# Kernel tuning notes

Hardware: AMD Instinct MI355X
Metric: run time of the kernel (lower is better)

The kernel has to match this reference:

```python
import jax, jax.numpy as jnp
import numpy as np

ATT_K = 180   # attention_k
NPOOL = 15    # WeldonPooling(15): mean of top-15 + mean of bottom-15 spatial scores


def setup_inputs() -> dict:
    key = jax.random.key(0)
    k1, k2, k3, k4 = jax.random.split(key, 4)
    imgs, emb, h, w = 16, 2400, 14, 14
    caps_cnt = 64
    return {
        "g": jax.random.normal(k1, (imgs, emb, h, w), dtype=jnp.float32),
        "caps": jax.random.normal(k2, (caps_cnt, emb), dtype=jnp.float32),
        "fc_w": jax.random.normal(k3, (emb, emb), dtype=jnp.float32) * 0.02,
        "fc_b": jax.random.normal(k4, (emb,), dtype=jnp.float32) * 0.02,
    }


def reference(g, caps, fc_w, fc_b):
    imgs, emb, h, w = g.shape
    caps_cnt = caps.shape[0]

    # ---- WeldonPooling(15): per (img, channel) sort spatial scores ----
    flat = g.reshape(imgs, emb, h * w)
    s = jnp.sort(flat, axis=2)  # ascending
    hpool = s[:, :, -NPOOL:].mean(axis=2) + s[:, :, :NPOOL].mean(axis=2)  # [imgs, emb]
    x = hpool @ fc_w.T + fc_b  # fc (dropout is identity at eval / p=0)

    # ---- get_heat_map: top-k caption dims, gather fc-projected features ----
    order = jnp.argsort(-caps, axis=1)[:, :ATT_K]                 # [C, k] indices
    vals = jnp.take_along_axis(caps, order, axis=1)               # [C, k] top-k values (desc)
    gf = jnp.einsum('oe,iehw->oihw', fc_w, g)                     # fc.weight @ g -> [emb, imgs, h, w]
    gsel = gf[order]                                              # gather -> [C, k, imgs, h, w]
    heat = jnp.sum(jnp.abs(gsel * vals[:, :, None, None, None]), axis=1)  # [C, imgs, h, w]
    heat = jnp.transpose(heat, (1, 0, 2, 3))                      # [imgs, C, h, w]
    heat = heat / jnp.sum(heat, axis=(2, 3), keepdims=True)       # normalize per (img, cap)

    # ---- attention_embedding: weighted spatial sum, then fc ----
    xa = jnp.einsum('ichw,iehw->ice', heat, g)                    # [imgs, C, emb]
    xa = xa @ fc_w.T + fc_b

    return x, xa, g
```

## Files before the change

kernel.cpp:

```cpp
#include <hip/hip_runtime.h>
#include <math.h>

#define IMGS 16
#define EMB 2400
#define HW 196
#define CAPS 64
#define ATTK 180
#define NPOOL 15
#define NCOLS (IMGS * HW)
#define KPAD 224

typedef __attribute__((ext_vector_type(8))) short short8;
typedef __attribute__((ext_vector_type(4))) float f32x4;
typedef const __attribute__((address_space(1))) unsigned int* gas1_t;
typedef __attribute__((address_space(3))) unsigned int* las3_t;
typedef unsigned long long ull;

__device__ inline unsigned short f2bf(float f) {
    unsigned int u = __builtin_bit_cast(unsigned int, f);
    u += 0x7fffu + ((u >> 16) & 1u);
    return (unsigned short)(u >> 16);
}
__device__ inline float bf2f(unsigned int lo16) {
    return __builtin_bit_cast(float, lo16 << 16);
}
__device__ inline unsigned f2sort(float f) {
    unsigned u = __builtin_bit_cast(unsigned, f);
    int msk = ((int)u) >> 31;
    return u ^ (unsigned)(msk | 0x80000000);
}


__device__ __forceinline__ void transpool_body(char* smem, int bx, int i,
                                               const float* __restrict__ g,
                                               float* __restrict__ hpool,
                                               unsigned short* __restrict__ gT,
                                               float* __restrict__ gout) {
    float(*t)[197] = (float(*)[197])smem;
    int e0 = bx * 32;
    int tid = threadIdx.x;
    const float* base = g + ((size_t)i * EMB + e0) * HW;
    float* obase = gout ? gout + ((size_t)i * EMB + e0) * HW : nullptr;
    for (int f = tid; f < 32 * HW; f += 256) {
        int e = f / HW, hw = f % HW;
        float v = base[(size_t)e * HW + hw];
        t[e][hw] = v;
        if (obase) obase[(size_t)e * HW + hw] = v;
    }
    __syncthreads();
    for (int f = tid; f < HW * 32; f += 256) {
        int hw = f / 32, e = f % 32;
        gT[((size_t)i * HW + hw) * EMB + e0 + e] = f2bf(t[e][hw]);
    }
    int w = tid >> 6, tl = tid & 63, hl = tl & 31;
    bool negh = tl >= 32;
#pragma unroll 1
    for (int rq = 0; rq < 2; ++rq) {
        int eb = w * 8 + rq * 4;
        float s[4][7];
#pragma unroll
        for (int r = 0; r < 4; r++) {
#pragma unroll
            for (int q = 0; q < 7; q++) {
                int hw = hl + 32 * q;
                if (hw < HW) {
                    unsigned u = __builtin_bit_cast(unsigned, t[eb + r][hw]);
                    if (negh) u ^= 0x80000000u;
                    s[r][q] = __builtin_bit_cast(
                        float, (u & 0xFFFFFF00u) | (unsigned)(q * 32 + hl));
                } else {
                    s[r][q] = -INFINITY;
                }
            }
        }
#define CS1(r, a, b)                                       \
    {                                                      \
        float hi = fmaxf(s[r][a], s[r][b]);                \
        float lo = fminf(s[r][a], s[r][b]);                \
        s[r][a] = hi; s[r][b] = lo;                        \
    }
#define CSQ(a, b) CS1(0, a, b) CS1(1, a, b) CS1(2, a, b) CS1(3, a, b)
        CSQ(1, 2) CSQ(3, 4) CSQ(5, 6)
        CSQ(0, 2) CSQ(3, 5) CSQ(4, 6)
        CSQ(0, 1) CSQ(4, 5) CSQ(2, 6)
        CSQ(0, 4) CSQ(1, 5)
        CSQ(0, 3) CSQ(2, 5)
        CSQ(1, 3) CSQ(2, 4)
        CSQ(2, 3)
#undef CSQ
#undef CS1
        float acc[4] = {0.f, 0.f, 0.f, 0.f};
#pragma unroll
        for (int it = 0; it < NPOOL; ++it) {
            int xx[4];
#pragma unroll
            for (int r = 0; r < 4; r++) xx[r] = __builtin_bit_cast(int, s[r][0]);
#define ST4(c)                                                                     \
    {                                                                              \
        _Pragma("unroll") for (int r = 0; r < 4; r++) {                            \
            int y = __builtin_amdgcn_update_dpp(xx[r], xx[r], c, 0xf, 0xf, false); \
            float a = fmaxf(__builtin_bit_cast(float, xx[r]),                      \
                            __builtin_bit_cast(float, y));                         \
            xx[r] = __builtin_bit_cast(int, a);                                    \
        }                                                                          \
    }
            ST4(0x111) ST4(0x112) ST4(0x114) ST4(0x118) ST4(0x142)
#undef ST4
#pragma unroll
            for (int r = 0; r < 4; r++) {
                int m31 = __builtin_amdgcn_readlane(xx[r], 31);
                int m63 = __builtin_amdgcn_readlane(xx[r], 63);
                float msel = __builtin_bit_cast(float, negh ? m63 : m31);
                acc[r] += msel;
                bool won = (__builtin_bit_cast(unsigned, s[r][0]) ==
                            __builtin_bit_cast(unsigned, msel));
                s[r][0] = won ? s[r][1] : s[r][0];
                s[r][1] = won ? s[r][2] : s[r][1];
                s[r][2] = won ? s[r][3] : s[r][2];
                s[r][3] = won ? s[r][4] : s[r][3];
                s[r][4] = won ? s[r][5] : s[r][4];
                s[r][5] = won ? s[r][6] : s[r][5];
                s[r][6] = won ? -INFINITY : s[r][6];
            }
        }
#pragma unroll
        for (int r = 0; r < 4; r++) {
            int ai = __builtin_bit_cast(int, acc[r]);
            float a0 = __builtin_bit_cast(float, __builtin_amdgcn_readlane(ai, 0));
            float a32 = __builtin_bit_cast(float, __builtin_amdgcn_readlane(ai, 32));
            if (tl == 0) hpool[(size_t)i * EMB + e0 + eb + r] = (a0 - a32) / 15.0f;
        }
    }
}

__device__ __forceinline__ void topk_body(char* smem, int c,
                                          const float* __restrict__ caps,
                                          int* __restrict__ idxs,
                                          float* __restrict__ vals) {
    float* rowf = (float*)smem;
    unsigned(*hist)[256] = (unsigned(*)[256])(smem + 9600);
    unsigned* scanbuf = (unsigned*)(smem + 13696);
    unsigned* wtot = (unsigned*)(smem + 14720);
    ull* sprefix = (ull*)(smem + 14744);
    int* srank = (int*)(smem + 14752);
    int tid = threadIdx.x;
    int w = tid >> 6, lane = tid & 63;
    const float4* src = (const float4*)(caps + (size_t)c * EMB);
    for (int j = tid; j < EMB / 4; j += 256) {
        float4 v = src[j];
        *(float4*)&rowf[j * 4] = v;
    }
    if (tid == 0) { *sprefix = 0ull; *srank = ATTK; }
#pragma unroll 1
    for (int pass = 0; pass < 6; ++pass) {
        __syncthreads();
        ull pref = *sprefix;
        int rk = *srank;
        int shift = 40 - pass * 8;
        ull pmaskhi = (pass == 0) ? 0ull : ~((1ull << (shift + 8)) - 1ull);
        hist[0][tid] = 0; hist[1][tid] = 0; hist[2][tid] = 0; hist[3][tid] = 0;
        __syncthreads();
        unsigned* myhist = hist[w];
#pragma unroll 1
        for (int s = 0; s < 10; s++) {
            int e = tid + s * 256;
            if (e < EMB) {
                ull key = ((ull)f2sort(rowf[e]) << 16) | ((unsigned)(2399 - e) << 4);
                if ((key & pmaskhi) == pref)
                    atomicAdd(&myhist[(unsigned)(key >> shift) & 255u], 1u);
            }
        }
        __syncthreads();
        unsigned h = hist[0][tid] + hist[1][tid] + hist[2][tid] + hist[3][tid];
        scanbuf[255 - tid] = h;
        __syncthreads();
        unsigned x = scanbuf[tid];
#pragma unroll
        for (int d = 1; d < 64; d <<= 1) {
            unsigned u = __shfl_up(x, d, 64);
            if (lane >= d) x += u;
        }
        if (lane == 63) wtot[w] = x;
        __syncthreads();
        unsigned off = 0;
        for (int ww = 0; ww < w; ww++) off += wtot[ww];
        scanbuf[tid] = x + off;
        __syncthreads();
        unsigned incl = scanbuf[255 - tid];
        unsigned excl = incl - h;
        if (h > 0u && excl < (unsigned)rk && incl >= (unsigned)rk) {
            *srank = rk - (int)excl;
            *sprefix = pref | ((ull)tid << shift);
        }
    }
    __syncthreads();
    ull T = *sprefix;
    unsigned selmask = 0, cnt = 0;
#pragma unroll 1
    for (int s = 0; s < 10; s++) {
        int e = tid + s * 256;
        if (e < EMB) {
            ull key = ((ull)f2sort(rowf[e]) << 16) | ((unsigned)(2399 - e) << 4);
            if (key >= T) { selmask |= 1u << s; cnt++; }
        }
    }
    unsigned x = cnt;
#pragma unroll
    for (int d = 1; d < 64; d <<= 1) {
        unsigned u = __shfl_up(x, d, 64);
        if (lane >= d) x += u;
    }
    if (lane == 63) wtot[w] = x;
    __syncthreads();
    unsigned off = 0;
    for (int ww = 0; ww < w; ww++) off += wtot[ww];
    unsigned slot = x + off - cnt;
#pragma unroll 1
    for (int s = 0; s < 10; s++) {
        if (selmask & (1u << s)) {
            int e = tid + s * 256;
            idxs[c * ATTK + slot] = e;
            vals[c * ATTK + slot] = fabsf(rowf[e]);
            slot++;
        }
    }
}

__device__ __forceinline__ void convw_body(int b, const float* __restrict__ fc_w,
                                           unsigned short* __restrict__ wbf) {
    int o = b * 4 + (threadIdx.x >> 6);
    int lane = threadIdx.x & 63;
    const float* wrow = fc_w + (size_t)o * EMB;
    unsigned short* wdst = wbf + (size_t)o * EMB;
    for (int e = lane * 4; e < EMB; e += 256) {
        float4 wv = *(const float4*)&wrow[e];
        ushort4 r;
        r.x = f2bf(wv.x); r.y = f2bf(wv.y); r.z = f2bf(wv.z); r.w = f2bf(wv.w);
        *(ushort4*)&wdst[e] = r;
    }
}

__global__ __launch_bounds__(256) void combo_kernel(const float* __restrict__ g,
                                                    float* __restrict__ hpool,
                                                    unsigned short* __restrict__ gT,
                                                    float* __restrict__ gout,
                                                    const float* __restrict__ caps,
                                                    int* __restrict__ idxs,
                                                    float* __restrict__ vals,
                                                    const float* __restrict__ fc_w,
                                                    unsigned short* __restrict__ wbf,
                                                    int nconv) {
    __shared__ __align__(16) char smem[25664];
    int b = blockIdx.x;
    constexpr int NTP = (EMB / 32) * IMGS;
    if (b < NTP) {
        transpool_body(smem, b % (EMB / 32), b / (EMB / 32), g, hpool, gT, gout);
    } else if (b < NTP + nconv) {
        convw_body(b - NTP, fc_w, wbf);
    } else {
        topk_body(smem, b - NTP - nconv, caps, idxs, vals);
    }
}

__global__ void x_kernel(const float* __restrict__ hpool, const float* __restrict__ fc_w,
                         const float* __restrict__ fc_b, float* __restrict__ x_out) {
    int o = blockIdx.x;
    int lane = threadIdx.x;
    float acc[IMGS];
#pragma unroll
    for (int i = 0; i < IMGS; i++) acc[i] = 0.f;
    const float* wrow = fc_w + (size_t)o * EMB;
    for (int e = lane; e < EMB; e += 64) {
        float wv = wrow[e];
#pragma unroll
        for (int i = 0; i < IMGS; i++) acc[i] += hpool[i * EMB + e] * wv;
    }
#pragma unroll
    for (int i = 0; i < IMGS; i++) {
#pragma unroll
        for (int sdx = 32; sdx > 0; sdx >>= 1) acc[i] += __shfl_xor(acc[i], sdx, 64);
    }
    if (lane == 0) {
        float bo = fc_b[o];
#pragma unroll
        for (int i = 0; i < IMGS; i++) x_out[i * EMB + o] = acc[i] + bo;
    }
}

template <int MF, int NF, int OUT_MODE>
__global__ __launch_bounds__(256) void gemm_gll(const unsigned short* __restrict__ A,
                                                const unsigned short* __restrict__ B,
                                                void* __restrict__ outp,
                                                const float* __restrict__ bias,
                                                const float* __restrict__ invS,
                                                int M, int N, int K, int ldb, int kper,
                                                long az, long bz) {
    constexpr int BM = MF * 32, BN = NF * 32;
    constexpr int ROWS = BM + BN;
    constexpr int RPAD = (ROWS + 63) & ~63;
    constexpr int NCALL = RPAD / 16;
    constexpr int LPW = NCALL / 4;
    __shared__ unsigned short lds[3][RPAD][32];
    int gx = gridDim.x, gy = gridDim.y;
    int nwg = gx * gy;
    int flat = blockIdx.y * gx + blockIdx.x;
    int qq = nwg >> 3, rr8 = nwg & 7;
    int xcd = flat & 7, idx = flat >> 3;
    int base = (xcd < rr8) ? xcd * (qq + 1) : rr8 * (qq + 1) + (xcd - rr8) * qq;
    int nf = base + idx;
    int m0 = (nf % gy) * BM;
    int n0 = (nf / gy) * BN;
    int z = blockIdx.z;
    const unsigned short* Ab = A + (size_t)z * az;
    const unsigned short* Bb = B + (size_t)z * bz;
    int kb = (az == 0 && bz == 0) ? z * kper : 0;
    int nt = kper / 32;
    int tid = threadIdx.x, w = tid >> 6, lane = tid & 63;
    int wm = (w >> 1) * (MF * 16), wn = (w & 1) * (NF * 16);
    int ln = lane & 15;
    int ks = (((lane >> 4) ^ ((lane >> 1) & 3))) * 8;
    int srow = lane >> 2;
    int skc = (((lane & 3) ^ ((lane >> 3) & 3))) * 8;

    auto STAGE = [&](int buf, int t) {
        int k0 = kb + t * 32;
#pragma unroll
        for (int j = 0; j < LPW; j++) {
            int jj = w + j * 4;
            int r = jj * 16 + srow;
            const unsigned short* src;
            if (r < BM) src = Ab + (size_t)(m0 + r) * K + k0 + skc;
            else if (r < ROWS) src = Bb + (size_t)(n0 + r - BM) * ldb + k0 + skc;
            else src = Ab + (size_t)m0 * K + k0 + skc;
            __builtin_amdgcn_global_load_lds((gas1_t)(const void*)src,
                                             (las3_t)(void*)&lds[buf][jj * 16][0], 16, 0, 0);
        }
    };

    STAGE(0, 0);
    if (nt > 1) STAGE(1, 1);
    f32x4 acc[MF][NF] = {};
    for (int t = 0; t < nt; ++t) {
        if (t + 1 < nt) {
            if constexpr (LPW == 4) asm volatile("s_waitcnt vmcnt(4) lgkmcnt(0)" ::: "memory");
            else if constexpr (LPW == 5) asm volatile("s_waitcnt vmcnt(5) lgkmcnt(0)" ::: "memory");
            else if constexpr (LPW == 6) asm volatile("s_waitcnt vmcnt(6) lgkmcnt(0)" ::: "memory");
            else asm volatile("s_waitcnt vmcnt(0) lgkmcnt(0)" ::: "memory");
        } else {
            asm volatile("s_waitcnt vmcnt(0) lgkmcnt(0)" ::: "memory");
        }
        __builtin_amdgcn_s_barrier();
        __builtin_amdgcn_sched_barrier(0);
        if (t + 2 < nt) STAGE((t + 2) % 3, t + 2);
        const unsigned short(*buf)[32] = lds[t % 3];
        short8 af[MF], bfv[NF];
#pragma unroll
        for (int mf = 0; mf < MF; mf++)
            af[mf] = *(const short8*)&buf[wm + mf * 16 + ln][ks];
#pragma unroll
        for (int nfi = 0; nfi < NF; nfi++)
            bfv[nfi] = *(const short8*)&buf[BM + wn + nfi * 16 + ln][ks];
        __builtin_amdgcn_s_setprio(1);
#pragma unroll
        for (int mf = 0; mf < MF; mf++)
#pragma unroll
            for (int nfi = 0; nfi < NF; nfi++)
                acc[mf][nfi] = __builtin_amdgcn_mfma_f32_16x16x32_bf16(af[mf], bfv[nfi],
                                                                       acc[mf][nfi], 0, 0, 0);
        __builtin_amdgcn_s_setprio(0);
    }
#pragma unroll
    for (int mf = 0; mf < MF; mf++) {
#pragma unroll
        for (int nfi = 0; nfi < NF; nfi++) {
#pragma unroll
            for (int rr = 0; rr < 4; rr++) {
                int row = m0 + wm + mf * 16 + (lane >> 4) * 4 + rr;
                int col = n0 + wn + nfi * 16 + ln;
                float v = acc[mf][nfi][rr];
                if (OUT_MODE == 6) {
                    ((unsigned short*)outp)[(size_t)row * N + col] = f2bf(v);
                } else if (OUT_MODE == 4) {
                    ((float*)outp)[((size_t)z * CAPS + row) * N + col] =
                        v * invS[z * CAPS + row] + bias[col];
                }
            }
        }
    }
}

__device__ inline uint4 load8(const unsigned short* p) { return *(const uint4*)p; }
__device__ inline uint4 load8(const float* p) {
    float4 a = *(const float4*)p;
    float4 b = *(const float4*)(p + 4);
    uint4 r;
    r.x = (unsigned)f2bf(a.x) | ((unsigned)f2bf(a.y) << 16);
    r.y = (unsigned)f2bf(a.z) | ((unsigned)f2bf(a.w) << 16);
    r.z = (unsigned)f2bf(b.x) | ((unsigned)f2bf(b.y) << 16);
    r.w = (unsigned)f2bf(b.z) | ((unsigned)f2bf(b.w) << 16);
    return r;
}

template <int MF, int NF, typename TA, typename TB>
__global__ __launch_bounds__(256) void mfma_gemm_nt(const TA* __restrict__ A,
                                                    const TB* __restrict__ B,
                                                    void* __restrict__ outp,
                                                    int M, int N, int K) {
    constexpr int BM = MF * 32, BN = NF * 32;
    constexpr int nA = BM * 4, nTot = (BM + BN) * 4;
    constexpr int NCH = (nTot + 255) / 256;
    __shared__ unsigned short As[BM][40];
    __shared__ unsigned short Bs[BN][40];
    int m0 = blockIdx.y * BM, n0 = blockIdx.x * BN;
    int tid = threadIdx.x;
    int w = tid >> 6, lane = tid & 63;
    int wm = (w >> 1) * (MF * 16), wn = (w & 1) * (NF * 16);
    int ln = lane & 15, ks = (lane >> 4) * 8;
    uint4 r[NCH];
#pragma unroll
    for (int j = 0; j < NCH; j++) {
        int c = tid + 256 * j;
        if (c < nTot) {
            if (c < nA) {
                int row = c >> 2, kc = c & 3;
                r[j] = load8(A + (size_t)(m0 + row) * K + kc * 8);
            } else {
                int cc = c - nA, row = cc >> 2, kc = cc & 3;
                r[j] = load8(B + (size_t)(n0 + row) * K + kc * 8);
            }
        }
    }
    f32x4 acc[MF][NF] = {};
    for (int k0 = 0; k0 < K; k0 += 32) {
#pragma unroll
        for (int j = 0; j < NCH; j++) {
            int c = tid + 256 * j;
            if (c < nTot) {
                if (c < nA) {
                    int row = c >> 2, kc = c & 3;
                    *(uint4*)&As[row][kc * 8] = r[j];
                } else {
                    int cc = c - nA, row = cc >> 2, kc = cc & 3;
                    *(uint4*)&Bs[row][kc * 8] = r[j];
                }
            }
        }
        __syncthreads();
        if (k0 + 32 < K) {
#pragma unroll
            for (int j = 0; j < NCH; j++) {
                int c = tid + 256 * j;
                if (c < nTot) {
                    if (c < nA) {
                        int row = c >> 2, kc = c & 3;
                        r[j] = load8(A + (size_t)(m0 + row) * K + (k0 + 32) + kc * 8);
                    } else {
                        int cc = c - nA, row = cc >> 2, kc = cc & 3;
                        r[j] = load8(B + (size_t)(n0 + row) * K + (k0 + 32) + kc * 8);
                    }
                }
            }
        }
        short8 af[MF], bfv[NF];
#pragma unroll
        for (int mf = 0; mf < MF; mf++)
            af[mf] = *(const short8*)&As[wm + mf * 16 + ln][ks];
#pragma unroll
        for (int nfi = 0; nfi < NF; nfi++)
            bfv[nfi] = *(const short8*)&Bs[wn + nfi * 16 + ln][ks];
#pragma unroll
        for (int mf = 0; mf < MF; mf++)
#pragma unroll
            for (int nfi = 0; nfi < NF; nfi++)
                acc[mf][nfi] = __builtin_amdgcn_mfma_f32_16x16x32_bf16(af[mf], bfv[nfi],
                                                                       acc[mf][nfi], 0, 0, 0);
        __syncthreads();
    }
#pragma unroll
    for (int mf = 0; mf < MF; mf++) {
#pragma unroll
        for (int nfi = 0; nfi < NF; nfi++) {
#pragma unroll
            for (int rr = 0; rr < 4; rr++) {
                int row = m0 + wm + mf * 16 + (lane >> 4) * 4 + rr;
                int col = n0 + wn + nfi * 16 + ln;
                ((unsigned short*)outp)[(size_t)row * N + col] = f2bf(acc[mf][nfi][rr]);
            }
        }
    }
}

__global__ __launch_bounds__(256) void heatx_kernel(const int* __restrict__ idxs,
                                                    const float* __restrict__ vals,
                                                    const unsigned short* __restrict__ A,
                                                    unsigned short* __restrict__ Hnbf,
                                                    float* __restrict__ invS,
                                                    const float* __restrict__ hpool,
                                                    const unsigned short* __restrict__ wbf,
                                                    const float* __restrict__ fc_b,
                                                    float* __restrict__ x_out,
                                                    int nheat) {
    __shared__ int sidx[ATTK];
    __shared__ float sval[ATTK];
    __shared__ float wsum[4];
    int b = blockIdx.x;
    int tid = threadIdx.x;
    int w = tid >> 6, lane = tid & 63;
    if (b < nheat) {
        int i = b % IMGS, c = b / IMGS;
        if (tid < ATTK) {
            sidx[tid] = idxs[c * ATTK + tid];
            sval[tid] = vals[c * ATTK + tid];
        }
        __syncthreads();
        int hw = tid;
        float v = 0.f;
        if (hw < HW) {
            int n = i * HW + hw;
            float a0 = 0.f, a1 = 0.f, a2 = 0.f, a3 = 0.f;
#pragma unroll 1
            for (int j = 0; j < ATTK; j += 4) {
                a0 += sval[j + 0] * bf2f(A[(size_t)sidx[j + 0] * NCOLS + n] & 0x7FFFu);
                a1 += sval[j + 1] * bf2f(A[(size_t)sidx[j + 1] * NCOLS + n] & 0x7FFFu);
                a2 += sval[j + 2] * bf2f(A[(size_t)sidx[j + 2] * NCOLS + n] & 0x7FFFu);
                a3 += sval[j + 3] * bf2f(A[(size_t)sidx[j + 3] * NCOLS + n] & 0x7FFFu);
            }
            v = (a0 + a1) + (a2 + a3);
        }
        if (hw < KPAD)
            Hnbf[((size_t)i * CAPS + c) * KPAD + hw] =
                (hw < HW) ? f2bf(v) : (unsigned short)0;
        float s = v;
#pragma unroll
        for (int d = 32; d > 0; d >>= 1) s += __shfl_xor(s, d, 64);
        if (lane == 0) wsum[w] = s;
        __syncthreads();
        if (tid == 0)
            invS[i * CAPS + c] = 1.0f / (wsum[0] + wsum[1] + wsum[2] + wsum[3]);
    } else {
        int o = (b - nheat) * 4 + w;
        float acc[IMGS];
#pragma unroll
        for (int i = 0; i < IMGS; i++) acc[i] = 0.f;
        const unsigned short* wrow = wbf + (size_t)o * EMB;
        for (int e = lane * 4; e < EMB; e += 256) {
            ushort4 wq = *(const ushort4*)&wrow[e];
            float w0 = bf2f(wq.x), w1 = bf2f(wq.y), w2 = bf2f(wq.z), w3 = bf2f(wq.w);
#pragma unroll
            for (int i = 0; i < IMGS; i++) {
                const float* hp = hpool + i * EMB + e;
                acc[i] += hp[0] * w0 + hp[1] * w1 + hp[2] * w2 + hp[3] * w3;
            }
        }
#pragma unroll
        for (int i = 0; i < IMGS; i++) {
#pragma unroll
            for (int sdx = 32; sdx > 0; sdx >>= 1) acc[i] += __shfl_xor(acc[i], sdx, 64);
        }
        if (lane == 0) {
            float bo = fc_b[o];
#pragma unroll
            for (int i = 0; i < IMGS; i++) x_out[i * EMB + o] = acc[i] + bo;
        }
    }
}

extern "C" void kernel_launch(void* const* d_in, const int* in_sizes, int n_in,
                              void* d_out, int out_size, void* d_ws, size_t ws_size,
                              hipStream_t stream) {
    const float* g = (const float*)d_in[0];
    const float* caps = (const float*)d_in[1];
    const float* fc_w = (const float*)d_in[2];
    const float* fc_b = (const float*)d_in[3];

    float* out = (float*)d_out;
    float* x_out = out;
    float* xa_out = out + 38400;
    float* g_out = out + 38400 + 2457600;

    float* ws = (float*)d_ws;
    float* hpool = ws;
    int* idxs = (int*)(ws + 38400);
    float* vals = ws + 49920;
    float* invS = ws + 61440;
    unsigned short* Hnbf = (unsigned short*)(ws + 62464);
    unsigned short* wbf = (unsigned short*)(ws + 1490944);
    bool use_wbf = ws_size >= (size_t)17483776;
    bool ws_big = use_wbf && ws_size >= (size_t)(17483776 + 2 * 15052800);
    unsigned short* gT_big = (unsigned short*)((char*)d_ws + 17483776);
    unsigned short* Asig_big = (unsigned short*)((char*)d_ws + 17483776 + 15052800);

    unsigned short* Asig = ws_big ? Asig_big : (unsigned short*)g_out;
    unsigned short* gT = ws_big ? gT_big : ((unsigned short*)g_out + (size_t)EMB * NCOLS);

    if (use_wbf) {
        combo_kernel<<<(EMB / 32) * IMGS + EMB / 4 + CAPS, 256, 0, stream>>>(
            g, hpool, gT, ws_big ? g_out : nullptr, caps, idxs, vals, fc_w, wbf, EMB / 4);
        gemm_gll<5, 7, 6><<<dim3(NCOLS / 224, EMB / 160, 1), 256, 0, stream>>>(
            wbf, gT, Asig, nullptr, nullptr, EMB, NCOLS, EMB, EMB, EMB, 0, 0);
        heatx_kernel<<<IMGS * CAPS + EMB / 4, 256, 0, stream>>>(
            idxs, vals, Asig, Hnbf, invS, hpool, wbf, fc_b, x_out, IMGS * CAPS);
    } else {
        combo_kernel<<<(EMB / 32) * IMGS + CAPS, 256, 0, stream>>>(
            g, hpool, gT, nullptr, caps, idxs, vals, fc_w, nullptr, 0);
        x_kernel<<<EMB, 64, 0, stream>>>(hpool, fc_w, fc_b, x_out);
        mfma_gemm_nt<5, 2, float, unsigned short>
            <<<dim3(NCOLS / 64, EMB / 160), 256, 0, stream>>>(fc_w, gT, Asig,
                                                              EMB, NCOLS, EMB);
        heatx_kernel<<<IMGS * CAPS, 256, 0, stream>>>(
            idxs, vals, Asig, Hnbf, invS, hpool, nullptr, fc_b, x_out, IMGS * CAPS);
    }
    gemm_gll<2, 5, 4><<<dim3(EMB / 160, 1, IMGS), 256, 0, stream>>>(
        Hnbf, Asig, xa_out, fc_b, invS, CAPS, EMB, KPAD, NCOLS, KPAD,
        (long)CAPS * KPAD, HW);
    if (!ws_big) {
        hipMemcpyAsync(g_out, g, sizeof(float) * (size_t)IMGS * EMB * HW,
                       hipMemcpyDeviceToDevice, stream);
    }
}
```

Measured before the change: 147.0 us.

## Split-K the large fc_w @ g GEMM in two with bf16 partial reduction

```diff
diff --git a/kernel.cpp b/kernel.cpp
--- a/kernel.cpp
+++ b/kernel.cpp
@@ -313,8 +313,16 @@
     int z = blockIdx.z;
     const unsigned short* Ab = A + (size_t)z * az;
     const unsigned short* Bb = B + (size_t)z * bz;
-    int kb = (az == 0 && bz == 0) ? z * kper : 0;
-    int nt = kper / 32;
+    int kb, nt;
+    if (az == 0 && bz == 0) {
+        kb = z * kper;
+        int kc = K - kb;
+        if (kc > kper) kc = kper;
+        nt = kc / 32;
+    } else {
+        kb = 0;
+        nt = kper / 32;
+    }
     int tid = threadIdx.x, w = tid >> 6, lane = tid & 63;
     int wm = (w >> 1) * (MF * 16), wn = (w & 1) * (NF * 16);
     int ln = lane & 15;
@@ -380,6 +388,9 @@
                 float v = acc[mf][nfi][rr];
                 if (OUT_MODE == 6) {
                     ((unsigned short*)outp)[(size_t)row * N + col] = f2bf(v);
+                } else if (OUT_MODE == 7) {
+                    ((unsigned short*)outp)[(size_t)z * M * N + (size_t)row * N + col] =
+                        f2bf(v);
                 } else if (OUT_MODE == 4) {
                     ((float*)outp)[((size_t)z * CAPS + row) * N + col] =
                         v * invS[z * CAPS + row] + bias[col];
@@ -387,6 +398,27 @@
             }
         }
     }
+}
+
+__global__ __launch_bounds__(256) void reduceA_kernel(unsigned short* pp) {
+    const size_t S = (size_t)EMB * NCOLS;
+    size_t i = ((size_t)blockIdx.x * 256 + threadIdx.x) * 8;
+    if (i >= S) return;
+    ushort4 a0 = *(const ushort4*)&pp[i];
+    ushort4 a1 = *(const ushort4*)&pp[i + 4];
+    ushort4 b0 = *(const ushort4*)&pp[S + i];
+    ushort4 b1 = *(const ushort4*)&pp[S + i + 4];
+    ushort4 r0, r1;
+    r0.x = f2bf(bf2f(a0.x) + bf2f(b0.x));
+    r0.y = f2bf(bf2f(a0.y) + bf2f(b0.y));
+    r0.z = f2bf(bf2f(a0.z) + bf2f(b0.z));
+    r0.w = f2bf(bf2f(a0.w) + bf2f(b0.w));
+    r1.x = f2bf(bf2f(a1.x) + bf2f(b1.x));
+    r1.y = f2bf(bf2f(a1.y) + bf2f(b1.y));
+    r1.z = f2bf(bf2f(a1.z) + bf2f(b1.z));
+    r1.w = f2bf(bf2f(a1.w) + bf2f(b1.w));
+    *(ushort4*)&pp[i] = r0;
+    *(ushort4*)&pp[i + 4] = r1;
 }
 
 __device__ inline uint4 load8(const unsigned short* p) { return *(const uint4*)p; }
@@ -578,6 +610,7 @@
     float* xa_out = out + 38400;
     float* g_out = out + 38400 + 2457600;
 
+    const size_t S = (size_t)EMB * NCOLS;
     float* ws = (float*)d_ws;
     float* hpool = ws;
     int* idxs = (int*)(ws + 38400);
@@ -587,17 +620,32 @@
     unsigned short* wbf = (unsigned short*)(ws + 1490944);
     bool use_wbf = ws_size >= (size_t)17483776;
     bool ws_big = use_wbf && ws_size >= (size_t)(17483776 + 2 * 15052800);
-    unsigned short* gT_big = (unsigned short*)((char*)d_ws + 17483776);
-    unsigned short* Asig_big = (unsigned short*)((char*)d_ws + 17483776 + 15052800);
-
-    unsigned short* Asig = ws_big ? Asig_big : (unsigned short*)g_out;
-    unsigned short* gT = ws_big ? gT_big : ((unsigned short*)g_out + (size_t)EMB * NCOLS);
+    bool ws_huge = use_wbf && ws_size >= (size_t)(17483776 + 3 * 15052800);
+
+    unsigned short* Asig;
+    unsigned short* gT;
+    if (ws_huge) {
+        Asig = (unsigned short*)((char*)d_ws + 17483776);
+        gT = Asig + 2 * S;
+    } else if (ws_big) {
+        gT = (unsigned short*)((char*)d_ws + 17483776);
+        Asig = gT + S;
+    } else {
+        Asig = (unsigned short*)g_out;
+        gT = Asig + S;
+    }
 
     if (use_wbf) {
         combo_kernel<<<(EMB / 32) * IMGS + EMB / 4 + CAPS, 256, 0, stream>>>(
             g, hpool, gT, ws_big ? g_out : nullptr, caps, idxs, vals, fc_w, wbf, EMB / 4);
-        gemm_gll<5, 7, 6><<<dim3(NCOLS / 224, EMB / 160, 1), 256, 0, stream>>>(
-            wbf, gT, Asig, nullptr, nullptr, EMB, NCOLS, EMB, EMB, EMB, 0, 0);
+        if (ws_huge) {
+            gemm_gll<5, 7, 7><<<dim3(NCOLS / 224, EMB / 160, 2), 256, 0, stream>>>(
+                wbf, gT, Asig, nullptr, nullptr, EMB, NCOLS, EMB, EMB, 1216, 0, 0);
+            reduceA_kernel<<<(int)(S / 8 / 256), 256, 0, stream>>>(Asig);
+        } else {
+            gemm_gll<5, 7, 6><<<dim3(NCOLS / 224, EMB / 160, 1), 256, 0, stream>>>(
+                wbf, gT, Asig, nullptr, nullptr, EMB, NCOLS, EMB, EMB, EMB, 0, 0);
+        }
         heatx_kernel<<<IMGS * CAPS + EMB / 4, 256, 0, stream>>>(
             idxs, vals, Asig, Hnbf, invS, hpool, wbf, fc_b, x_out, IMGS * CAPS);
     } else {
```

Result: slower. 158.2 us (+7.6%).
